# Kernel optimization log

Measured on AMD Instinct MI355X. Metric: run time of the kernel, lower is better.

The kernel has to match this reference:

```python
import jax, jax.numpy as jnp
import numpy as np

PAD = 2  # F.conv2d(padding=2) with 5x5 kernels -> SAME

def setup_inputs() -> dict:
    key = jax.random.key(0)
    k1, k2 = jax.random.split(key)
    B, H, W, C = 64, 128, 128, 3
    KH, KW, N = 5, 5, 10  # last_frames(2) * num_transformed_images(5)
    images = jax.random.uniform(k1, (B, H, W, C), dtype=jnp.float32)
    kernels = jax.random.uniform(k2, (B, KH, KW, N), dtype=jnp.float32)
    return {"images": images, "kernels": kernels}


def reference(images, kernels):
    """Faithful JAX version of apply_cdna_kernels.

    images:  [B, H, W, C]
    kernels: [B, KH, KW, N]
    returns: [N, B, C, H, W] (the torch code returns N split tensors of
             shape [1, B, C, H, W]; we return the equivalent stacked array).
    Implemented as a single grouped cross-correlation with
    feature_group_count=B, fusing the per-batch F.conv2d loop.
    """
    B, H, W, C = images.shape
    _, KH, KW, N = kernels.shape
    # torch: images.permute([3,0,1,2]) -> [C, B, H, W]; treat C as conv batch,
    # B as input channels, one input channel per group.
    inp = jnp.transpose(images, (3, 0, 1, 2))  # [C, B, H, W]
    # weights: group b owns output channels b*N:(b+1)*N, each 1 input channel
    w = jnp.transpose(kernels, (0, 3, 1, 2)).reshape(B * N, 1, KH, KW)
    out = jax.lax.conv_general_dilated(
        inp, w,
        window_strides=(1, 1),
        padding=((PAD, PAD), (PAD, PAD)),
        feature_group_count=B,
        dimension_numbers=("NCHW", "OIHW", "NCHW"),
    )  # [C, B*N, H, W]
    out = out.reshape(C, B, N, H, W)
    return jnp.transpose(out, (2, 1, 0, 3, 4))  # [N, B, C, H, W]
```

## Files before the change

kernel.cpp:

```cpp
#include <hip/hip_runtime.h>


#define B_  64
#define H_  128
#define W_  128
#define C_  3
#define N_  10
#define KH_ 5
#define KW_ 5
#define TH_ 8
#define LDS_ROWS (TH_ + 4)
#define ROW_F ((W_ + 4) * C_)
#define ROW_VALID (W_ * C_)
#define HW_ (H_ * W_)

__device__ __forceinline__ float uni(float x) {
    return __int_as_float(__builtin_amdgcn_readfirstlane(__float_as_int(x)));
}

__global__ __launch_bounds__(256, 2) void cdna_apply_kernel(
    const float* __restrict__ images,
    const float* __restrict__ kernels,
    float* __restrict__ out)
{
    __shared__ __align__(16) float s_img[LDS_ROWS * ROW_F];

    const int tid = threadIdx.x;
    const int ht  = blockIdx.x;
    const int b   = blockIdx.y;
    const int y0  = ht * TH_;

    const float* __restrict__ ib = images + (long)b * (H_ * W_ * C_);
    for (int i = tid; i < LDS_ROWS * (ROW_F / 4); i += 256) {
        const int r  = i / (ROW_F / 4);
        const int q  = i - r * (ROW_F / 4);
        const int y  = y0 + r - 2;
        float v0 = 0.f, v1 = 0.f, v2 = 0.f, v3 = 0.f;
        if ((unsigned)y < (unsigned)H_) {
            const float* grow = ib + (long)y * ROW_VALID;
            const int f0 = q * 4 - 6;
            if (f0 >= 0 && f0 <= ROW_VALID - 4) {
                const float2 a  = *(const float2*)(grow + f0);
                const float2 c2 = *(const float2*)(grow + f0 + 2);
                v0 = a.x; v1 = a.y; v2 = c2.x; v3 = c2.y;
            } else {
                if (f0 + 0 >= 0 && f0 + 0 < ROW_VALID) v0 = grow[f0 + 0];
                if (f0 + 1 >= 0 && f0 + 1 < ROW_VALID) v1 = grow[f0 + 1];
                if (f0 + 2 >= 0 && f0 + 2 < ROW_VALID) v2 = grow[f0 + 2];
                if (f0 + 3 >= 0 && f0 + 3 < ROW_VALID) v3 = grow[f0 + 3];
            }
        }
        *(float4*)(&s_img[r * ROW_F + q * 4]) = make_float4(v0, v1, v2, v3);
    }
    __syncthreads();

    const int tx = tid & 31;
    const int ty = tid >> 5;

    const float* __restrict__ kb = kernels + (long)b * (KH_ * KW_ * N_);
    const int h = y0 + ty;
    float* ob0 = out + (long)b * (C_ * HW_) + (long)h * W_ + tx * 4;
    const long nstride = (long)B_ * C_ * HW_;

    #pragma unroll 1
    for (int np = 0; np < N_ / 2; ++np) {
        const int n0 = 2 * np;
        float wt0[KH_ * KW_], wt1[KH_ * KW_];
        #pragma unroll
        for (int k = 0; k < KH_ * KW_; ++k) {
            wt0[k] = uni(kb[k * N_ + n0]);
            wt1[k] = uni(kb[k * N_ + n0 + 1]);
        }

        float a0[12], a1[12];
        #pragma unroll
        for (int i = 0; i < 12; ++i) { a0[i] = 0.f; a1[i] = 0.f; }

        #pragma unroll
        for (int r = 0; r < KH_; ++r) {
            const float4* rp = (const float4*)&s_img[(ty + r) * ROW_F + tx * 12];
            float px[24];
            #pragma unroll
            for (int j = 0; j < 6; ++j) {
                const float4 t = rp[j];
                px[j * 4 + 0] = t.x; px[j * 4 + 1] = t.y;
                px[j * 4 + 2] = t.z; px[j * 4 + 3] = t.w;
            }
            #pragma unroll
            for (int kw = 0; kw < KW_; ++kw) {
                const float w0 = wt0[r * KW_ + kw];
                const float w1 = wt1[r * KW_ + kw];
                #pragma unroll
                for (int w = 0; w < 4; ++w)
                    #pragma unroll
                    for (int c = 0; c < C_; ++c) {
                        const float p = px[(kw + w) * 3 + c];
                        a0[c * 4 + w] = fmaf(p, w0, a0[c * 4 + w]);
                        a1[c * 4 + w] = fmaf(p, w1, a1[c * 4 + w]);
                    }
            }
        }

        float* p0 = ob0 + (long)n0 * nstride;
        float* p1 = p0 + nstride;
        #pragma unroll
        for (int c = 0; c < C_; ++c) {
            *(float4*)(p0 + (long)c * HW_) = make_float4(a0[c*4+0], a0[c*4+1], a0[c*4+2], a0[c*4+3]);
            *(float4*)(p1 + (long)c * HW_) = make_float4(a1[c*4+0], a1[c*4+1], a1[c*4+2], a1[c*4+3]);
        }
    }
}

extern "C" void kernel_launch(void* const* d_in, const int* in_sizes, int n_in,
                              void* d_out, int out_size, void* d_ws, size_t ws_size,
                              hipStream_t stream) {
    const float* images  = (const float*)d_in[0];
    const float* kernels = (const float*)d_in[1];
    float* out = (float*)d_out;

    dim3 grid(H_ / TH_, B_);
    cdna_apply_kernel<<<grid, 256, 0, stream>>>(images, kernels, out);
}
```

Before: 144.7 us.

## Split output channels across block halves with smaller row tiles

Halves the row tile to 4 rows and splits the 256 threads into two groups. One group computes channel pairs 0-5 and the other pairs 6-9, so each block covers 4 rows instead of 8 and the grid doubles. Weights are now loaded per kernel row inside a non-unrolled loop instead of all 50 up front, which cuts register pressure so occupancy can rise to 3 blocks per CU. The costs are load imbalance (3 pairs vs 2 per group), a larger halo-to-interior ratio when staging rows into LDS, and more repeated weight loads.

```diff
diff --git a/kernel.cpp b/kernel.cpp
--- a/kernel.cpp
+++ b/kernel.cpp
@@ -8,17 +8,13 @@
 #define N_  10
 #define KH_ 5
 #define KW_ 5
-#define TH_ 8
+#define TH_ 4
 #define LDS_ROWS (TH_ + 4)
 #define ROW_F ((W_ + 4) * C_)
 #define ROW_VALID (W_ * C_)
 #define HW_ (H_ * W_)
 
-__device__ __forceinline__ float uni(float x) {
-    return __int_as_float(__builtin_amdgcn_readfirstlane(__float_as_int(x)));
-}
-
-__global__ __launch_bounds__(256, 2) void cdna_apply_kernel(
+__global__ __launch_bounds__(256, 3) void cdna_apply_kernel(
     const float* __restrict__ images,
     const float* __restrict__ kernels,
     float* __restrict__ out)
@@ -55,29 +51,33 @@
     __syncthreads();
 
     const int tx = tid & 31;
-    const int ty = tid >> 5;
+    const int ty = (tid >> 5) & 3;
+    const int s  = __builtin_amdgcn_readfirstlane(tid >> 7);
 
     const float* __restrict__ kb = kernels + (long)b * (KH_ * KW_ * N_);
     const int h = y0 + ty;
     float* ob0 = out + (long)b * (C_ * HW_) + (long)h * W_ + tx * 4;
     const long nstride = (long)B_ * C_ * HW_;
 
+    const int pmax = 3 - s;
+
     #pragma unroll 1
-    for (int np = 0; np < N_ / 2; ++np) {
-        const int n0 = 2 * np;
-        float wt0[KH_ * KW_], wt1[KH_ * KW_];
-        #pragma unroll
-        for (int k = 0; k < KH_ * KW_; ++k) {
-            wt0[k] = uni(kb[k * N_ + n0]);
-            wt1[k] = uni(kb[k * N_ + n0 + 1]);
-        }
+    for (int p = 0; p < pmax; ++p) {
+        const int n0 = 2 * p + 6 * s;
 
         float a0[12], a1[12];
         #pragma unroll
         for (int i = 0; i < 12; ++i) { a0[i] = 0.f; a1[i] = 0.f; }
 
-        #pragma unroll
+        #pragma unroll 1
         for (int r = 0; r < KH_; ++r) {
+            float w0[KW_], w1[KW_];
+            #pragma unroll
+            for (int kw = 0; kw < KW_; ++kw) {
+                w0[kw] = kb[(r * KW_ + kw) * N_ + n0];
+                w1[kw] = kb[(r * KW_ + kw) * N_ + n0 + 1];
+            }
+
             const float4* rp = (const float4*)&s_img[(ty + r) * ROW_F + tx * 12];
             float px[24];
             #pragma unroll
@@ -86,17 +86,18 @@
                 px[j * 4 + 0] = t.x; px[j * 4 + 1] = t.y;
                 px[j * 4 + 2] = t.z; px[j * 4 + 3] = t.w;
             }
+
             #pragma unroll
             for (int kw = 0; kw < KW_; ++kw) {
-                const float w0 = wt0[r * KW_ + kw];
-                const float w1 = wt1[r * KW_ + kw];
+                const float g0 = w0[kw];
+                const float g1 = w1[kw];
                 #pragma unroll
                 for (int w = 0; w < 4; ++w)
                     #pragma unroll
                     for (int c = 0; c < C_; ++c) {
-                        const float p = px[(kw + w) * 3 + c];
-                        a0[c * 4 + w] = fmaf(p, w0, a0[c * 4 + w]);
-                        a1[c * 4 + w] = fmaf(p, w1, a1[c * 4 + w]);
+                        const float pv = px[(kw + w) * 3 + c];
+                        a0[c * 4 + w] = fmaf(pv, g0, a0[c * 4 + w]);
+                        a1[c * 4 + w] = fmaf(pv, g1, a1[c * 4 + w]);
                     }
             }
         }
```

Result: no change. 143.4 us (-0.9%).
